# Optimization experiments

Measured on AMD Instinct MI355X. Metric: run time of the kernel, lower is better.

## Reference

```python
import jax, jax.numpy as jnp
import numpy as np
import math

D = 1024
B, S = 4, 4096


def setup_inputs() -> dict:
    key = jax.random.key(0)
    ks = jax.random.split(key, 8)
    x = jax.random.normal(ks[0], (B, S, D), dtype=jnp.float32)
    W_omega = jax.random.normal(ks[1], (D, D), dtype=jnp.float32) * (1.0 / math.sqrt(D))
    b_omega = jnp.zeros((D,), dtype=jnp.float32)
    log_scale = jnp.full((D,), math.log(0.1), dtype=jnp.float32)
    ln_gamma = jnp.ones((4 * D,), dtype=jnp.float32)
    ln_beta = jnp.zeros((4 * D,), dtype=jnp.float32)
    W1 = jax.random.normal(ks[2], (4 * D, 2 * D), dtype=jnp.float32) * (1.0 / math.sqrt(4 * D))
    b1 = jnp.zeros((2 * D,), dtype=jnp.float32)
    W2 = jax.random.normal(ks[3], (2 * D, D), dtype=jnp.float32) * (1.0 / math.sqrt(2 * D))
    b2 = jnp.zeros((D,), dtype=jnp.float32)
    return {"x": x, "W_omega": W_omega, "b_omega": b_omega, "log_scale": log_scale,
            "ln_gamma": ln_gamma, "ln_beta": ln_beta, "W1": W1, "b1": b1, "W2": W2, "b2": b2}


def _layernorm(x, gamma, beta, eps=1e-5):
    mu = jnp.mean(x, axis=-1, keepdims=True)
    var = jnp.var(x, axis=-1, keepdims=True)
    return (x - mu) * jax.lax.rsqrt(var + eps) * gamma + beta


def reference(x, W_omega, b_omega, log_scale, ln_gamma, ln_beta, W1, b1, W2, b2):
    # x: (B, S, D)
    seq_len = x.shape[1]
    omega = jnp.einsum('bsd,de->bse', x, W_omega) + b_omega
    position = jnp.arange(1, seq_len + 1, dtype=x.dtype)[None, :, None]  # (1,S,1)
    pos_scale = 1.0 / jnp.sqrt(position)
    scale = jnp.exp(log_scale)
    omega_scaled = omega * scale * pos_scale
    phi = jnp.cumsum(omega_scaled, axis=1)
    cos_phi = jnp.cos(phi)
    sin_phi = jnp.sin(phi)
    content_real = x * cos_phi
    content_imag = x * sin_phi
    mem_real = jnp.cumsum(content_real, axis=1) / position
    mem_imag = jnp.cumsum(content_imag, axis=1) / position
    retrieved_real = mem_real * cos_phi + mem_imag * sin_phi
    retrieved_imag = mem_imag * cos_phi - mem_real * sin_phi
    context = jnp.concatenate([content_real, content_imag, retrieved_real, retrieved_imag], axis=-1)
    h = _layernorm(context, ln_gamma, ln_beta)
    h = jnp.einsum('bsf,fg->bsg', h, W1) + b1
    h = jax.nn.gelu(h, approximate=False)  # torch GELU default is exact erf
    # dropout is identity in eval mode
    phase_contribution = jnp.einsum('bsg,gd->bsd', h, W2) + b2
    return x + phase_contribution
```

## Files before the change

kernel.cpp:

```cpp
#include <hip/hip_runtime.h>
#include <hip/hip_bf16.h>
#include <math.h>

typedef __hip_bfloat16 bf16;
typedef __attribute__((ext_vector_type(8))) short bf16x8;
typedef __attribute__((ext_vector_type(4))) float f32x4;

static constexpr int DD = 1024;
static constexpr int BB = 4;
static constexpr int SS = 4096;
static constexpr int FD = 4096;
static constexpr int GDIM = 2048;
static constexpr long SD = (long)SS * DD;
static constexpr long SD4 = 4 * SD;

__device__ __forceinline__ void gl2lds16(const bf16* g, bf16* l) {
    __builtin_amdgcn_global_load_lds(
        (const __attribute__((address_space(1))) void*)g,
        (__attribute__((address_space(3))) void*)l, 16, 0, 0);
}

template <int EPI>
__global__ __launch_bounds__(512, 2) void gemm256(
    const bf16* __restrict__ A, const bf16* __restrict__ BT, void* __restrict__ Cp,
    const float* __restrict__ bias, const float* __restrict__ Xadd,
    int M, int N, int K, long strA, long strBT, long strC)
{
    extern __shared__ bf16 lds[];
    const int tid = threadIdx.x;
    const int l = tid & 63, wv = tid >> 6;
    const int wr = wv >> 2, wc = wv & 3;

    int lin = blockIdx.y * gridDim.x + blockIdx.x;
    {
        const int nwg = gridDim.x * gridDim.y;
        const int qq = nwg >> 3, rr = nwg & 7;
        const int xcd = lin & 7, idx = lin >> 3;
        lin = (xcd < rr ? xcd * (qq + 1) : rr * (qq + 1) + (xcd - rr) * qq) + idx;
    }
    const long m0 = (long)(lin / gridDim.x) * 256;
    const long n0 = (long)(lin % gridDim.x) * 256;

    A += (long)blockIdx.z * strA;
    BT += (long)blockIdx.z * strBT;

    const int schunk = (tid & 3) ^ ((tid >> 3) & 3);
    const bf16* pa = A + (m0 + (tid >> 2)) * (long)K + schunk * 8;
    const bf16* pb = BT + (n0 + (tid >> 2)) * (long)K + schunk * 8;
    const long rowK = 128L * (long)K;
    const int stgOff = wv * 512;

    const int fm = l & 15, q = l >> 4;
    const int lof = fm * 32 + ((q ^ ((fm >> 1) & 3)) * 8);

    f32x4 acc[8][4];
#pragma unroll
    for (int i = 0; i < 8; ++i)
#pragma unroll
        for (int j = 0; j < 4; ++j) acc[i][j] = (f32x4){0.f, 0.f, 0.f, 0.f};

    const int NT = K >> 6;

    {
        bf16* dA0 = lds + stgOff;
        bf16* dB0 = lds + 32768 + stgOff;
        bf16* dA1 = lds + 8192 + stgOff;
        bf16* dB1 = lds + 40960 + stgOff;
        gl2lds16(pa, dA0);       gl2lds16(pa + rowK, dA0 + 4096);
        gl2lds16(pb, dB0);       gl2lds16(pb + rowK, dB0 + 4096);
        gl2lds16(pa + 32, dA1);  gl2lds16(pa + 32 + rowK, dA1 + 4096);
        gl2lds16(pb + 32, dB1);  gl2lds16(pb + 32 + rowK, dB1 + 4096);
        asm volatile("s_waitcnt vmcnt(4)" ::: "memory");
        __builtin_amdgcn_s_barrier();
    }

    bf16x8 af[4], bq[4];
    for (int t = 0; t < NT; ++t) {
        const int buf = t & 1;
        const bool more = (t + 1) < NT;
        const long ko = (long)(t + 1) * 64;
        const bf16* As0 = lds + (buf << 1) * 8192;
        const bf16* As1 = As0 + 8192;
        const bf16* Bs0 = lds + 32768 + (buf << 1) * 8192;
        const bf16* Bs1 = Bs0 + 8192;
        bf16* nA0 = lds + ((buf ^ 1) << 1) * 8192 + stgOff;
        bf16* nA1 = nA0 + 8192;
        bf16* nB0 = lds + 32768 + ((buf ^ 1) << 1) * 8192 + stgOff;
        bf16* nB1 = nB0 + 8192;

        {
            const bf16* bb = Bs0 + (wc * 64) * 32 + lof;
            const bf16* ab = As0 + (wr * 128) * 32 + lof;
#pragma unroll
            for (int j = 0; j < 4; ++j) bq[j] = *(const bf16x8*)(bb + j * 512);
#pragma unroll
            for (int i = 0; i < 4; ++i) af[i] = *(const bf16x8*)(ab + i * 512);
            if (more) { gl2lds16(pa + ko, nA0); gl2lds16(pa + ko + rowK, nA0 + 4096); }
            __builtin_amdgcn_s_barrier();
            asm volatile("s_waitcnt lgkmcnt(0)" ::: "memory");
            __builtin_amdgcn_s_setprio(1);
#pragma unroll
            for (int i = 0; i < 4; ++i)
#pragma unroll
                for (int j = 0; j < 4; ++j)
                    acc[i][j] = __builtin_amdgcn_mfma_f32_16x16x32_bf16(af[i], bq[j], acc[i][j], 0, 0, 0);
            __builtin_amdgcn_s_setprio(0);
            __builtin_amdgcn_s_barrier();
        }
        {
            const bf16* ab = As0 + (wr * 128 + 64) * 32 + lof;
#pragma unroll
            for (int i = 0; i < 4; ++i) af[i] = *(const bf16x8*)(ab + i * 512);
            if (more) {
                gl2lds16(pb + ko, nB0); gl2lds16(pb + ko + rowK, nB0 + 4096);
                asm volatile("s_waitcnt vmcnt(4)" ::: "memory");
            } else {
                asm volatile("s_waitcnt vmcnt(0)" ::: "memory");
            }
            __builtin_amdgcn_s_barrier();
            asm volatile("s_waitcnt lgkmcnt(0)" ::: "memory");
            __builtin_amdgcn_s_setprio(1);
#pragma unroll
            for (int i = 0; i < 4; ++i)
#pragma unroll
                for (int j = 0; j < 4; ++j)
                    acc[4 + i][j] = __builtin_amdgcn_mfma_f32_16x16x32_bf16(af[i], bq[j], acc[4 + i][j], 0, 0, 0);
            __builtin_amdgcn_s_setprio(0);
            __builtin_amdgcn_s_barrier();
        }
        {
            const bf16* bb = Bs1 + (wc * 64) * 32 + lof;
            const bf16* ab = As1 + (wr * 128) * 32 + lof;
#pragma unroll
            for (int j = 0; j < 4; ++j) bq[j] = *(const bf16x8*)(bb + j * 512);
#pragma unroll
            for (int i = 0; i < 4; ++i) af[i] = *(const bf16x8*)(ab + i * 512);
            if (more) { gl2lds16(pa + ko + 32, nA1); gl2lds16(pa + ko + 32 + rowK, nA1 + 4096); }
            __builtin_amdgcn_s_barrier();
            asm volatile("s_waitcnt lgkmcnt(0)" ::: "memory");
            __builtin_amdgcn_s_setprio(1);
#pragma unroll
            for (int i = 0; i < 4; ++i)
#pragma unroll
                for (int j = 0; j < 4; ++j)
                    acc[i][j] = __builtin_amdgcn_mfma_f32_16x16x32_bf16(af[i], bq[j], acc[i][j], 0, 0, 0);
            __builtin_amdgcn_s_setprio(0);
            __builtin_amdgcn_s_barrier();
        }
        {
            const bf16* ab = As1 + (wr * 128 + 64) * 32 + lof;
#pragma unroll
            for (int i = 0; i < 4; ++i) af[i] = *(const bf16x8*)(ab + i * 512);
            if (more) {
                gl2lds16(pb + ko + 32, nB1); gl2lds16(pb + ko + 32 + rowK, nB1 + 4096);
                asm volatile("s_waitcnt vmcnt(4)" ::: "memory");
            }
            __builtin_amdgcn_s_barrier();
            asm volatile("s_waitcnt lgkmcnt(0)" ::: "memory");
            __builtin_amdgcn_s_setprio(1);
#pragma unroll
            for (int i = 0; i < 4; ++i)
#pragma unroll
                for (int j = 0; j < 4; ++j)
                    acc[4 + i][j] = __builtin_amdgcn_mfma_f32_16x16x32_bf16(af[i], bq[j], acc[4 + i][j], 0, 0, 0);
            __builtin_amdgcn_s_setprio(0);
            __builtin_amdgcn_s_barrier();
        }
    }

    const long cb = (long)blockIdx.z * strC;
#pragma unroll
    for (int i = 0; i < 8; ++i) {
        const long rB = m0 + wr * 128 + i * 16 + q * 4;
#pragma unroll
        for (int j = 0; j < 4; ++j) {
            const long col = n0 + wc * 64 + j * 16 + fm;
#pragma unroll
            for (int r2 = 0; r2 < 4; ++r2) {
                const long row = rB + r2;
                float v = acc[i][j][r2];
                if (EPI == 0) {
                    v += bias[row];
                    ((bf16*)Cp)[cb + row * (long)N + col] = __float2bfloat16(v);
                } else if (EPI == 1) {
                    v += bias[col];
                    v = 0.5f * v * (1.0f + erff(v * 0.70710678118654752f));
                    ((bf16*)Cp)[cb + row * (long)N + col] = __float2bfloat16(v);
                } else {
                    v += bias[col] + Xadd[row * (long)N + col];
                    ((float*)Cp)[cb + row * (long)N + col] = v;
                }
            }
        }
    }
}

__global__ void conv_bf16(const float* __restrict__ in, bf16* __restrict__ out, long n) {
    long i = ((long)blockIdx.x * 256 + threadIdx.x) * 4;
    if (i >= n) return;
    const float4 v = *(const float4*)(in + i);
    bf16 o[4] = {__float2bfloat16(v.x), __float2bfloat16(v.y),
                 __float2bfloat16(v.z), __float2bfloat16(v.w)};
    *(uint2*)(out + i) = *(uint2*)o;
}

__global__ void transpose_f32_bf16(const float* __restrict__ in, bf16* __restrict__ out,
                                   int R, int C, long inStr, long outStr) {
    __shared__ float tl[64][65];
    const float* ip = in + (long)blockIdx.z * inStr;
    bf16* op = out + (long)blockIdx.z * outStr;
    const int r0 = blockIdx.y * 64, c0 = blockIdx.x * 64;
    const int tr = threadIdx.x >> 6, tc = threadIdx.x & 63;
#pragma unroll
    for (int k = 0; k < 16; k++) {
        int r = k * 4 + tr;
        tl[r][tc] = ip[(long)(r0 + r) * C + c0 + tc];
    }
    __syncthreads();
#pragma unroll
    for (int k = 0; k < 16; k++) {
        int r = k * 4 + tr;
        op[(long)(c0 + r) * R + r0 + tc] = __float2bfloat16(tl[tc][r]);
    }
}

__global__ __launch_bounds__(256) void scan_kernel(
    const bf16* __restrict__ omegaT, const bf16* __restrict__ xT,
    const float* __restrict__ log_scale, bf16* __restrict__ ctx,
    long strIn, long strCtx)
{
    const int d = blockIdx.x * 4 + (threadIdx.x >> 6);
    const int lane = threadIdx.x & 63;
    const float sc = expf(log_scale[d]);
    const bf16* po = omegaT + (long)blockIdx.z * strIn + (long)d * SS;
    const bf16* px = xT + (long)blockIdx.z * strIn + (long)d * SS;
    bf16* pc = ctx + (long)blockIdx.z * strCtx + (long)d * SS;

    float phi_c = 0.f, mr_c = 0.f, mi_c = 0.f;
    for (int tchunk = 0; tchunk < SS / 64; tchunk++) {
        const int s = tchunk * 64 + lane;
        const float pos = (float)(s + 1);
        float w = __bfloat162float(po[s]) * sc * rsqrtf(pos);
#pragma unroll
        for (int dlt = 1; dlt < 64; dlt <<= 1) {
            float v = __shfl_up(w, dlt, 64);
            if (lane >= dlt) w += v;
        }
        const float phi = phi_c + w;
        float sph, cph;
        sincosf(phi, &sph, &cph);
        const float xv = __bfloat162float(px[s]);
        const float cr = xv * cph, ci = xv * sph;
        float crs = cr, cis = ci;
#pragma unroll
        for (int dlt = 1; dlt < 64; dlt <<= 1) {
            float v1 = __shfl_up(crs, dlt, 64);
            float v2 = __shfl_up(cis, dlt, 64);
            if (lane >= dlt) { crs += v1; cis += v2; }
        }
        const float invp = 1.0f / pos;
        const float mr = (mr_c + crs) * invp;
        const float mi = (mi_c + cis) * invp;
        const float rr = mr * cph + mi * sph;
        const float ri = mi * cph - mr * sph;
        pc[s] = __float2bfloat16(cr);
        pc[(long)DD * SS + s] = __float2bfloat16(ci);
        pc[2L * DD * SS + s] = __float2bfloat16(rr);
        pc[3L * DD * SS + s] = __float2bfloat16(ri);
        phi_c += __shfl(w, 63, 64);
        mr_c += __shfl(crs, 63, 64);
        mi_c += __shfl(cis, 63, 64);
    }
}

__global__ void zero_f32(float* p, int n) {
    int i = blockIdx.x * 256 + threadIdx.x;
    if (i < n) p[i] = 0.f;
}

__global__ void stats_kernel(const bf16* __restrict__ ctx, float* __restrict__ sums,
                             float* __restrict__ sqs) {
    const int s = blockIdx.x * 256 + threadIdx.x;
    const int f0 = blockIdx.y * 512;
    const int z = blockIdx.z;
    const bf16* p = ctx + (long)z * SD4 + (long)f0 * SS + s;
    float sm = 0.f, sq = 0.f;
    for (int f = 0; f < 512; f++) {
        float v = __bfloat162float(p[(long)f * SS]);
        sm += v;
        sq += v * v;
    }
    atomicAdd(&sums[z * SS + s], sm);
    atomicAdd(&sqs[z * SS + s], sq);
}

__global__ __launch_bounds__(256) void lnt_pair(
    bf16* __restrict__ ctx, const float* __restrict__ sums, const float* __restrict__ sqs,
    const float* __restrict__ gamma, const float* __restrict__ beta)
{
    __shared__ float tA[64][65];
    __shared__ float tB[64][65];
    const int z = blockIdx.z;
    int rem = blockIdx.x, a = 0;
    for (int i = 0; i < 64; i++) {
        int cnt = 64 - i;
        if (rem < cnt) { a = i; break; }
        rem -= cnt;
    }
    const int b = a + rem;
    bf16* base = ctx + (long)z * SD4;
    const int tr = threadIdx.x >> 6, tc = threadIdx.x & 63;
    const float* sums_z = sums + z * SS;
    const float* sqs_z = sqs + z * SS;

#pragma unroll
    for (int k = 0; k < 16; k++) {
        int i = k * 4 + tr;
        tA[i][tc] = __bfloat162float(base[(long)(a * 64 + i) * SS + b * 64 + tc]);
    }
    if (a != b) {
#pragma unroll
        for (int k = 0; k < 16; k++) {
            int i = k * 4 + tr;
            tB[i][tc] = __bfloat162float(base[(long)(b * 64 + i) * SS + a * 64 + tc]);
        }
    }
    __syncthreads();

    {
        const float g = gamma[a * 64 + tc], be = beta[a * 64 + tc];
#pragma unroll
        for (int k = 0; k < 16; k++) {
            const int i = k * 4 + tr;
            const int s = b * 64 + i;
            const float mu = sums_z[s] * (1.0f / FD);
            const float var = sqs_z[s] * (1.0f / FD) - mu * mu;
            const float is = rsqrtf(var + 1e-5f);
            const float v = (tA[tc][i] - mu) * is * g + be;
            base[(long)s * FD + a * 64 + tc] = __float2bfloat16(v);
        }
    }
    if (a != b) {
        const float g = gamma[b * 64 + tc], be = beta[b * 64 + tc];
#pragma unroll
        for (int k = 0; k < 16; k++) {
            const int i = k * 4 + tr;
            const int s = a * 64 + i;
            const float mu = sums_z[s] * (1.0f / FD);
            const float var = sqs_z[s] * (1.0f / FD) - mu * mu;
            const float is = rsqrtf(var + 1e-5f);
            const float v = (tB[tc][i] - mu) * is * g + be;
            base[(long)s * FD + b * 64 + tc] = __float2bfloat16(v);
        }
    }
}

extern "C" void kernel_launch(void* const* d_in, const int* in_sizes, int n_in,
                              void* d_out, int out_size, void* d_ws, size_t ws_size,
                              hipStream_t stream)
{
    const float* x = (const float*)d_in[0];
    const float* Wo = (const float*)d_in[1];
    const float* bo = (const float*)d_in[2];
    const float* lsc = (const float*)d_in[3];
    const float* gam = (const float*)d_in[4];
    const float* bet = (const float*)d_in[5];
    const float* W1 = (const float*)d_in[6];
    const float* b1 = (const float*)d_in[7];
    const float* W2 = (const float*)d_in[8];
    const float* b2 = (const float*)d_in[9];

    static bool attr_done = false;
    if (!attr_done) {
        hipFuncSetAttribute(reinterpret_cast<const void*>(gemm256<0>),
                            hipFuncAttributeMaxDynamicSharedMemorySize, 131072);
        hipFuncSetAttribute(reinterpret_cast<const void*>(gemm256<1>),
                            hipFuncAttributeMaxDynamicSharedMemorySize, 131072);
        hipFuncSetAttribute(reinterpret_cast<const void*>(gemm256<2>),
                            hipFuncAttributeMaxDynamicSharedMemorySize, 131072);
        attr_done = true;
    }

    char* ws = (char*)d_ws;
    const size_t MB = 1024 * 1024;

    bf16* W1T = (bf16*)(ws + 0);
    bf16* W2T = (bf16*)(ws + 16 * MB);
    bf16* WoT = (bf16*)(ws + 20 * MB);
    float* sums = (float*)(ws + 22 * MB);
    float* sqs = sums + 4 * SS;

    transpose_f32_bf16<<<dim3(DD / 64, DD / 64, 1), 256, 0, stream>>>(Wo, WoT, DD, DD, 0, 0);
    transpose_f32_bf16<<<dim3(GDIM / 64, FD / 64, 1), 256, 0, stream>>>(W1, W1T, FD, GDIM, 0, 0);
    transpose_f32_bf16<<<dim3(DD / 64, GDIM / 64, 1), 256, 0, stream>>>(W2, W2T, GDIM, DD, 0, 0);

    const int NPAIR = 64 * 65 / 2;

    if (ws_size >= 220 * MB) {
        bf16* xT  = (bf16*)(ws + 23 * MB);
        bf16* omT = (bf16*)(ws + 55 * MB);
        bf16* ctx = (bf16*)(ws + 87 * MB);
        bf16* xb  = (bf16*)(ws + 87 * MB);
        bf16* h1  = (bf16*)(ws + 23 * MB);

        conv_bf16<<<(int)(BB * SD / 1024), 256, 0, stream>>>(x, xb, BB * SD);
        transpose_f32_bf16<<<dim3(DD / 64, SS / 64, BB), 256, 0, stream>>>(x, xT, SS, DD, SD, SD);

        gemm256<0><<<dim3(SS / 256, DD / 256, BB), 512, 131072, stream>>>(
            WoT, xb, omT, bo, nullptr, DD, SS, DD, 0L, SD, SD);

        scan_kernel<<<dim3(DD / 4, 1, BB), 256, 0, stream>>>(omT, xT, lsc, ctx, SD, SD4);

        zero_f32<<<(8 * SS + 255) / 256, 256, 0, stream>>>(sums, 8 * SS);
        stats_kernel<<<dim3(SS / 256, FD / 512, BB), 256, 0, stream>>>(ctx, sums, sqs);

        lnt_pair<<<dim3(NPAIR, 1, BB), 256, 0, stream>>>(ctx, sums, sqs, gam, bet);

        gemm256<1><<<dim3(GDIM / 256, BB * SS / 256, 1), 512, 131072, stream>>>(
            ctx, W1T, h1, b1, nullptr, BB * SS, GDIM, FD, 0L, 0L, 0L);

        gemm256<2><<<dim3(DD / 256, BB * SS / 256, 1), 512, 131072, stream>>>(
            h1, W2T, d_out, b2, x, BB * SS, DD, GDIM, 0L, 0L, 0L);
    } else {
        bf16* xb  = (bf16*)(ws + 23 * MB);
        bf16* ctx = (bf16*)(ws + 23 * MB);
        bf16* omT = (bf16*)(ws + 55 * MB);
        bf16* xT  = (bf16*)(ws + 63 * MB);
        bf16* h1  = (bf16*)(ws + 55 * MB);

        for (int b = 0; b < BB; b++) {
            const float* xbf = x + (long)b * SD;
            conv_bf16<<<(int)(SD / 1024), 256, 0, stream>>>(xbf, xb, SD);
            transpose_f32_bf16<<<dim3(DD / 64, SS / 64, 1), 256, 0, stream>>>(xbf, xT, SS, DD, 0, 0);
            gemm256<0><<<dim3(SS / 256, DD / 256, 1), 512, 131072, stream>>>(
                WoT, xb, omT, bo, nullptr, DD, SS, DD, 0L, 0L, 0L);
            scan_kernel<<<dim3(DD / 4, 1, 1), 256, 0, stream>>>(omT, xT, lsc, ctx, 0L, 0L);
            zero_f32<<<(2 * SS + 255) / 256, 256, 0, stream>>>(sums, 2 * SS);
            stats_kernel<<<dim3(SS / 256, FD / 512, 1), 256, 0, stream>>>(ctx, sums, sqs);
            lnt_pair<<<dim3(NPAIR, 1, 1), 256, 0, stream>>>(ctx, sums, sqs, gam, bet);
            gemm256<1><<<dim3(GDIM / 256, SS / 256, 1), 512, 131072, stream>>>(
                ctx, W1T, h1, b1, nullptr, SS, GDIM, FD, 0L, 0L, 0L);
            gemm256<2><<<dim3(DD / 256, SS / 256, 1), 512, 131072, stream>>>(
                h1, W2T, (float*)d_out + (long)b * SD, b2, xbf, SS, DD, GDIM, 0L, 0L, 0L);
        }
    }
}
```

Baseline: 732.4 us.

## Cut GEMM main-loop barriers from eight to two per iteration

Restructures the 256-tile bf16 GEMM main loop so each k-half loads both A sub-tiles (a0, a1) from LDS up front and issues all of its global-to-LDS prefetches together. Only one vmcnt wait plus barrier remains per half, in place of the barrier pairs around every quarter. This cuts synchronisation stalls and lets the MFMA chains run back to back, at the cost of more live fragment registers and a changed wait/prefetch ordering that has to stay race-free across the double buffer.

```diff
diff --git a/kernel.cpp b/kernel.cpp
--- a/kernel.cpp
+++ b/kernel.cpp
@@ -63,8 +63,8 @@
 
     {
         bf16* dA0 = lds + stgOff;
+        bf16* dA1 = lds + 8192 + stgOff;
         bf16* dB0 = lds + 32768 + stgOff;
-        bf16* dA1 = lds + 8192 + stgOff;
         bf16* dB1 = lds + 40960 + stgOff;
         gl2lds16(pa, dA0);       gl2lds16(pa + rowK, dA0 + 4096);
         gl2lds16(pb, dB0);       gl2lds16(pb + rowK, dB0 + 4096);
@@ -74,96 +74,81 @@
         __builtin_amdgcn_s_barrier();
     }
 
-    bf16x8 af[4], bq[4];
     for (int t = 0; t < NT; ++t) {
         const int buf = t & 1;
         const bool more = (t + 1) < NT;
         const long ko = (long)(t + 1) * 64;
-        const bf16* As0 = lds + (buf << 1) * 8192;
+        const bf16* As0 = lds + buf * 16384;
         const bf16* As1 = As0 + 8192;
-        const bf16* Bs0 = lds + 32768 + (buf << 1) * 8192;
+        const bf16* Bs0 = lds + 32768 + buf * 16384;
         const bf16* Bs1 = Bs0 + 8192;
-        bf16* nA0 = lds + ((buf ^ 1) << 1) * 8192 + stgOff;
+        bf16* nA0 = lds + (buf ^ 1) * 16384 + stgOff;
         bf16* nA1 = nA0 + 8192;
-        bf16* nB0 = lds + 32768 + ((buf ^ 1) << 1) * 8192 + stgOff;
+        bf16* nB0 = lds + 32768 + (buf ^ 1) * 16384 + stgOff;
         bf16* nB1 = nB0 + 8192;
 
         {
             const bf16* bb = Bs0 + (wc * 64) * 32 + lof;
             const bf16* ab = As0 + (wr * 128) * 32 + lof;
+            bf16x8 bq[4], a0[4], a1[4];
 #pragma unroll
             for (int j = 0; j < 4; ++j) bq[j] = *(const bf16x8*)(bb + j * 512);
 #pragma unroll
-            for (int i = 0; i < 4; ++i) af[i] = *(const bf16x8*)(ab + i * 512);
-            if (more) { gl2lds16(pa + ko, nA0); gl2lds16(pa + ko + rowK, nA0 + 4096); }
-            __builtin_amdgcn_s_barrier();
-            asm volatile("s_waitcnt lgkmcnt(0)" ::: "memory");
+            for (int i = 0; i < 4; ++i) a0[i] = *(const bf16x8*)(ab + i * 512);
+#pragma unroll
+            for (int i = 0; i < 4; ++i) a1[i] = *(const bf16x8*)(ab + 64 * 32 + i * 512);
+            if (more) {
+                gl2lds16(pa + ko, nA0); gl2lds16(pa + ko + rowK, nA0 + 4096);
+                gl2lds16(pb + ko, nB0); gl2lds16(pb + ko + rowK, nB0 + 4096);
+            }
             __builtin_amdgcn_s_setprio(1);
 #pragma unroll
             for (int i = 0; i < 4; ++i)
 #pragma unroll
                 for (int j = 0; j < 4; ++j)
-                    acc[i][j] = __builtin_amdgcn_mfma_f32_16x16x32_bf16(af[i], bq[j], acc[i][j], 0, 0, 0);
+                    acc[i][j] = __builtin_amdgcn_mfma_f32_16x16x32_bf16(a0[i], bq[j], acc[i][j], 0, 0, 0);
             __builtin_amdgcn_s_setprio(0);
-            __builtin_amdgcn_s_barrier();
-        }
-        {
-            const bf16* ab = As0 + (wr * 128 + 64) * 32 + lof;
-#pragma unroll
-            for (int i = 0; i < 4; ++i) af[i] = *(const bf16x8*)(ab + i * 512);
-            if (more) {
-                gl2lds16(pb + ko, nB0); gl2lds16(pb + ko + rowK, nB0 + 4096);
-                asm volatile("s_waitcnt vmcnt(4)" ::: "memory");
-            } else {
-                asm volatile("s_waitcnt vmcnt(0)" ::: "memory");
-            }
-            __builtin_amdgcn_s_barrier();
-            asm volatile("s_waitcnt lgkmcnt(0)" ::: "memory");
+            if (more) { gl2lds16(pa + ko + 32, nA1); gl2lds16(pa + ko + 32 + rowK, nA1 + 4096); }
             __builtin_amdgcn_s_setprio(1);
 #pragma unroll
             for (int i = 0; i < 4; ++i)
 #pragma unroll
                 for (int j = 0; j < 4; ++j)
-                    acc[4 + i][j] = __builtin_amdgcn_mfma_f32_16x16x32_bf16(af[i], bq[j], acc[4 + i][j], 0, 0, 0);
+                    acc[4 + i][j] = __builtin_amdgcn_mfma_f32_16x16x32_bf16(a1[i], bq[j], acc[4 + i][j], 0, 0, 0);
             __builtin_amdgcn_s_setprio(0);
-            __builtin_amdgcn_s_barrier();
-        }
+        }
+        if (more) asm volatile("s_waitcnt vmcnt(6)" ::: "memory");
+        else      asm volatile("s_waitcnt vmcnt(0)" ::: "memory");
+        __builtin_amdgcn_s_barrier();
+
         {
             const bf16* bb = Bs1 + (wc * 64) * 32 + lof;
             const bf16* ab = As1 + (wr * 128) * 32 + lof;
+            bf16x8 bq[4], a0[4], a1[4];
 #pragma unroll
             for (int j = 0; j < 4; ++j) bq[j] = *(const bf16x8*)(bb + j * 512);
 #pragma unroll
-            for (int i = 0; i < 4; ++i) af[i] = *(const bf16x8*)(ab + i * 512);
-            if (more) { gl2lds16(pa + ko + 32, nA1); gl2lds16(pa + ko + 32 + rowK, nA1 + 4096); }
-            __builtin_amdgcn_s_barrier();
-            asm volatile("s_waitcnt lgkmcnt(0)" ::: "memory");
+            for (int i = 0; i < 4; ++i) a0[i] = *(const bf16x8*)(ab + i * 512);
+#pragma unroll
+            for (int i = 0; i < 4; ++i) a1[i] = *(const bf16x8*)(ab + 64 * 32 + i * 512);
+            if (more) { gl2lds16(pb + ko + 32, nB1); gl2lds16(pb + ko + 32 + rowK, nB1 + 4096); }
             __builtin_amdgcn_s_setprio(1);
 #pragma unroll
             for (int i = 0; i < 4; ++i)
 #pragma unroll
                 for (int j = 0; j < 4; ++j)
-                    acc[i][j] = __builtin_amdgcn_mfma_f32_16x16x32_bf16(af[i], bq[j], acc[i][j], 0, 0, 0);
+                    acc[i][j] = __builtin_amdgcn_mfma_f32_16x16x32_bf16(a0[i], bq[j], acc[i][j], 0, 0, 0);
             __builtin_amdgcn_s_setprio(0);
-            __builtin_amdgcn_s_barrier();
-        }
-        {
-            const bf16* ab = As1 + (wr * 128 + 64) * 32 + lof;
-#pragma unroll
-            for (int i = 0; i < 4; ++i) af[i] = *(const bf16x8*)(ab + i * 512);
-            if (more) {
-                gl2lds16(pb + ko + 32, nB1); gl2lds16(pb + ko + 32 + rowK, nB1 + 4096);
-                asm volatile("s_waitcnt vmcnt(4)" ::: "memory");
-            }
-            __builtin_amdgcn_s_barrier();
-            asm volatile("s_waitcnt lgkmcnt(0)" ::: "memory");
             __builtin_amdgcn_s_setprio(1);
 #pragma unroll
             for (int i = 0; i < 4; ++i)
 #pragma unroll
                 for (int j = 0; j < 4; ++j)
-                    acc[4 + i][j] = __builtin_amdgcn_mfma_f32_16x16x32_bf16(af[i], bq[j], acc[4 + i][j], 0, 0, 0);
+                    acc[4 + i][j] = __builtin_amdgcn_mfma_f32_16x16x32_bf16(a1[i], bq[j], acc[4 + i][j], 0, 0, 0);
             __builtin_amdgcn_s_setprio(0);
+        }
+        if (more) {
+            asm volatile("s_waitcnt vmcnt(4)" ::: "memory");
             __builtin_amdgcn_s_barrier();
         }
     }
```

Measured after the change: 756.0 us. 3.2% more time.
